# Kernel optimization log

Hardware: AMD Instinct MI355X
Metric: run time of the kernel (lower is better)

The kernel has to match this reference:

```python
import jax, jax.numpy as jnp
import numpy as np

N_NODES = 50000

def _spmm(edge_index, edge_weight, feat):
    # adj @ feat where adj is given as COO edge list (dst <- src)
    src = edge_index[1]
    dst = edge_index[0]
    msgs = feat[src] * edge_weight[:, None]  # [E, F]
    return jax.ops.segment_sum(msgs, dst, num_segments=N_NODES)

def setup_inputs() -> dict:
    key = jax.random.key(0)
    ks = jax.random.split(key, 8)
    E = 1600000
    x = jax.random.normal(ks[0], (N_NODES, 512), dtype=jnp.float32)
    edge_index = jax.random.randint(ks[1], (2, E), 0, N_NODES, dtype=jnp.int32)
    edge_weight = jax.random.uniform(ks[2], (E,), dtype=jnp.float32)
    # Glorot-ish init like GraphConvolution.reset_parameters
    W1 = jax.random.normal(ks[3], (512, 128), dtype=jnp.float32) / np.sqrt(512)
    b1 = jax.random.normal(ks[4], (128,), dtype=jnp.float32) * 0.01
    W2 = jax.random.normal(ks[5], (128, 64), dtype=jnp.float32) / np.sqrt(128)
    b2 = jax.random.normal(ks[6], (64,), dtype=jnp.float32) * 0.01
    return {"x": x, "edge_index": edge_index, "edge_weight": edge_weight,
            "W1": W1, "b1": b1, "W2": W2, "b2": b2}

def reference(x, edge_index, edge_weight, W1, b1, W2, b2):
    # eval mode: F.dropout is identity when not training
    # gc1: adj @ (x @ W1) + b1, then relu
    support1 = x @ W1                                   # [N, nhid]
    x1 = jax.nn.relu(_spmm(edge_index, edge_weight, support1) + b1)
    # gc2: adj @ (x1 @ W2) + b2
    support2 = x1 @ W2                                  # [N, out]
    x2 = _spmm(edge_index, edge_weight, support2) + b2
    return (x1, x2)
```

## Files before the change

kernel.cpp:

```cpp
#include <hip/hip_runtime.h>
#include <hip/hip_bf16.h>

#define N_NODES 50000
#define N_EDGES 1600000
#define F_IN    512
#define F_HID   128
#define F_OUT   64
#define NBUK    391
#define EPB     8192
#define CAP     4864

typedef short bf16x8 __attribute__((ext_vector_type(8)));
typedef float f32x4  __attribute__((ext_vector_type(4)));

__device__ __forceinline__ short f32_to_bf16(float f) {
    unsigned u = __float_as_uint(f);
    u += 0x7FFF + ((u >> 16) & 1);
    return (short)(u >> 16);
}
__device__ __forceinline__ float bf16_to_f32(short s) {
    return __uint_as_float(((unsigned)(unsigned short)s) << 16);
}
__device__ __forceinline__ float bf16lo(unsigned u) { return __uint_as_float(u << 16); }
__device__ __forceinline__ float bf16hi(unsigned u) { return __uint_as_float(u & 0xFFFF0000u); }

__device__ __forceinline__ bf16x8 cvt8(float4 lo, float4 hi) {
    union { unsigned u[4]; bf16x8 v; } r;
    asm("v_cvt_pk_bf16_f32 %0, %1, %2" : "=v"(r.u[0]) : "v"(lo.x), "v"(lo.y));
    asm("v_cvt_pk_bf16_f32 %0, %1, %2" : "=v"(r.u[1]) : "v"(lo.z), "v"(lo.w));
    asm("v_cvt_pk_bf16_f32 %0, %1, %2" : "=v"(r.u[2]) : "v"(hi.x), "v"(hi.y));
    asm("v_cvt_pk_bf16_f32 %0, %1, %2" : "=v"(r.u[3]) : "v"(hi.z), "v"(hi.w));
    return r.v;
}

__device__ __forceinline__ void gload16(const void* g, void* l) {
    __builtin_amdgcn_global_load_lds((const __attribute__((address_space(1))) void*)g,
                                     (__attribute__((address_space(3))) void*)l, 16, 0, 0);
}


__global__ __launch_bounds__(256) void part_a(const int* __restrict__ dst,
                                              const int* __restrict__ src,
                                              const float* __restrict__ w,
                                              int* __restrict__ gcnt,
                                              uint2* __restrict__ tmp, int E) {
    __shared__ int h[NBUK];
    __shared__ int base[NBUK];
    for (int i = threadIdx.x; i < NBUK; i += 256) h[i] = 0;
    __syncthreads();
    int e0 = blockIdx.x * EPB;
    int e1 = min(e0 + EPB, E);
    for (int e = e0 + threadIdx.x; e < e1; e += 256)
        atomicAdd(&h[dst[e] >> 7], 1);
    __syncthreads();
    for (int i = threadIdx.x; i < NBUK; i += 256) {
        int c = h[i];
        base[i] = c ? atomicAdd(&gcnt[i], c) : 0;
        h[i] = 0;
    }
    __syncthreads();
    for (int e = e0 + threadIdx.x; e < e1; e += 256) {
        int d = dst[e];
        int b = d >> 7;
        int off = base[b] + atomicAdd(&h[b], 1);
        if (off < CAP)
            tmp[(size_t)b * CAP + off] = make_uint2(((unsigned)d << 16) | (unsigned)src[e],
                                                    __float_as_uint(w[e]));
    }
}

__global__ __launch_bounds__(256) void part_b(const uint2* __restrict__ tmp,
                                              const int* __restrict__ gcnt,
                                              int2* __restrict__ rowinfo,
                                              uint2* __restrict__ erec) {
    __shared__ int s[128];
    __shared__ int cur[128];
    int b = blockIdx.x, tid = threadIdx.x;
    int nb0 = b << 7;
    int r0 = b * CAP;
    int cnt_b = min(gcnt[b], CAP);
    int r1 = r0 + cnt_b;
    if (tid < 128) s[tid] = 0;
    __syncthreads();
    for (int i = r0 + tid; i < r1; i += 256)
        atomicAdd(&s[(tmp[i].x >> 16) - nb0], 1);
    __syncthreads();
    int v = (tid < 128) ? s[tid] : 0;
    #pragma unroll
    for (int off = 1; off < 128; off <<= 1) {
        int t = (tid >= off && tid < 128) ? s[tid - off] : 0;
        __syncthreads();
        if (tid < 128) s[tid] += t;
        __syncthreads();
    }
    if (tid < 128) {
        int ex = r0 + s[tid] - v;
        cur[tid] = ex;
        int node = nb0 + tid;
        if (node < N_NODES) rowinfo[node] = make_int2(ex, ex + v);
    }
    __syncthreads();
    for (int i = r0 + tid; i < r1; i += 256) {
        uint2 rec = tmp[i];
        int p = atomicAdd(&cur[(rec.x >> 16) - nb0], 1);
        erec[p] = make_uint2(rec.x & 0xFFFFu, rec.y);
    }
}


template<int KD, int NC>
__global__ void wtrans_frag(const float* __restrict__ W, bf16x8* __restrict__ Bfrag) {
    constexpr int KC = KD / 32, NT = NC / 16;
    int u = blockIdx.x * 256 + threadIdx.x;
    if (u >= KC * NT * 64) return;
    int lane = u & 63;
    int nt   = (u >> 6) % NT;
    int kc   = u / (64 * NT);
    int n = nt * 16 + (lane & 15);
    int k = kc * 32 + (lane >> 4) * 8;
    bf16x8 f;
    #pragma unroll
    for (int j = 0; j < 8; ++j) f[j] = f32_to_bf16(W[(size_t)(k + j) * NC + n]);
    Bfrag[u] = f;
}

template<int KD , int NC >
__global__ __launch_bounds__(256) void mfma_gemm_s1(const float* __restrict__ X,
                                                    const bf16x8* __restrict__ Bfrag,
                                                    short* __restrict__ C, int Mrows) {
    constexpr int S = KD / 32;
    __shared__ char lds[2][16384];
    const int tid  = threadIdx.x;
    const int lane = tid & 63;
    const int wave = tid >> 6;
    const int wm = wave >> 1, wn = wave & 1;
    const int B0 = blockIdx.x * 64;
    const int r_lo = lane & 15, cg = lane >> 4;

    int rowA = B0 + wave * 16 + r_lo;
    if (rowA > Mrows - 1) rowA = Mrows - 1;
    const char* gA = (const char*)(X + (size_t)rowA * KD) + cg * 32;
    const char* gB = (const char*)Bfrag + (size_t)(wave * 2) * 1024 + (size_t)lane * 16;

    const int dA0 = (0 * 256 + wave * 64) * 16;
    const int dA1 = (1 * 256 + wave * 64) * 16;
    const int dB0 = 8192 + (wave * 2 + 0) * 1024;
    const int dB1 = 8192 + (wave * 2 + 1) * 1024;

    f32x4 acc[2][4];
    #pragma unroll
    for (int m = 0; m < 2; ++m)
        #pragma unroll
        for (int n = 0; n < 4; ++n) acc[m][n] = (f32x4){0.f, 0.f, 0.f, 0.f};

    {
        char* L = lds[0];
        gload16(gA,        L + dA0);
        gload16(gA + 16,   L + dA1);
        gload16(gB,        L + dB0);
        gload16(gB + 1024, L + dB1);
    }
    __syncthreads();

    int buf = 0;
    for (int s = 0; s < S; ++s) {
        if (s + 1 < S) {
            char* L = lds[buf ^ 1];
            const char* a = gA + (size_t)(s + 1) * 128;
            const char* b = gB + (size_t)(s + 1) * 8192;
            gload16(a,        L + dA0);
            gload16(a + 16,   L + dA1);
            gload16(b,        L + dB0);
            gload16(b + 1024, L + dB1);
        }
        const char* A_ = lds[buf];
        const char* B_ = lds[buf] + 8192;
        bf16x8 bb[4];
        #pragma unroll
        for (int n = 0; n < 4; ++n)
            bb[n] = *(const bf16x8*)(B_ + (wn * 4 + n) * 1024 + lane * 16);
        #pragma unroll
        for (int m = 0; m < 2; ++m) {
            int t = wm * 2 + m;
            float4 lo = *(const float4*)(A_ + (0 * 256 + t * 64 + lane) * 16);
            float4 hi = *(const float4*)(A_ + (1 * 256 + t * 64 + lane) * 16);
            bf16x8 a = cvt8(lo, hi);
            #pragma unroll
            for (int n = 0; n < 4; ++n)
                acc[m][n] = __builtin_amdgcn_mfma_f32_16x16x32_bf16(a, bb[n], acc[m][n], 0, 0, 0);
        }
        __syncthreads();
        buf ^= 1;
    }

    #pragma unroll
    for (int m = 0; m < 2; ++m) {
        int tile16 = (B0 >> 4) + wm * 2 + m;
        if (tile16 * 16 < Mrows) {
            #pragma unroll
            for (int n = 0; n < 4; ++n) {
                #pragma unroll
                for (int r = 0; r < 4; ++r) {
                    int grow = tile16 * 16 + cg * 4 + r;
                    C[(size_t)grow * NC + (wn * 4 + n) * 16 + r_lo] = f32_to_bf16(acc[m][n][r]);
                }
            }
        }
    }
}


template<int NC, int KD>
__global__ __launch_bounds__(256) void mfma_gemm_frag(const bf16x8* __restrict__ Afrag,
                                                      const bf16x8* __restrict__ Bfrag,
                                                      short* __restrict__ C, int Mt) {
    constexpr int NT = NC / 16, KC = KD / 32;
    constexpr int PFA = (KC < 4) ? KC : 4;
    const int lane = threadIdx.x & 63;
    const int wave = threadIdx.x >> 6;
    const int tile = blockIdx.x * 4 + wave;
    if (tile >= Mt) return;

    const bf16x8* ap = Afrag + (size_t)tile * KC * 64 + lane;
    const bf16x8* bp = Bfrag + lane;

    f32x4 acc[NT];
    #pragma unroll
    for (int i = 0; i < NT; ++i) acc[i] = (f32x4){0.f, 0.f, 0.f, 0.f};

    bf16x8 abuf[PFA];
    #pragma unroll
    for (int i = 0; i < PFA; ++i) abuf[i] = ap[(size_t)i * 64];
    bf16x8 bbuf[NT];
    #pragma unroll
    for (int nt = 0; nt < NT; ++nt) bbuf[nt] = bp[(size_t)nt * 64];

    #pragma unroll
    for (int kc = 0; kc < KC; ++kc) {
        bf16x8 a = abuf[kc % PFA];
        int ka = kc + PFA; if (ka > KC - 1) ka = KC - 1;
        abuf[kc % PFA] = ap[(size_t)ka * 64];
        int kb = (kc + 1 < KC) ? kc + 1 : kc;
        bf16x8 bnew[NT];
        #pragma unroll
        for (int nt = 0; nt < NT; ++nt) {
            bnew[nt] = bp[((size_t)kb * NT + nt) * 64];
            acc[nt] = __builtin_amdgcn_mfma_f32_16x16x32_bf16(a, bbuf[nt], acc[nt], 0, 0, 0);
        }
        #pragma unroll
        for (int nt = 0; nt < NT; ++nt) bbuf[nt] = bnew[nt];
    }

    const int lrow = lane & 15, kgrp = lane >> 4;
    #pragma unroll
    for (int nt = 0; nt < NT; ++nt) {
        #pragma unroll
        for (int r = 0; r < 4; ++r) {
            int grow = tile * 16 + kgrp * 4 + r;
            C[(size_t)grow * NC + nt * 16 + lrow] = f32_to_bf16(acc[nt][r]);
        }
    }
}


__global__ __launch_bounds__(64) void spmm128(const int2* __restrict__ rowinfo,
                                              const uint2* __restrict__ erec,
                                              const unsigned* __restrict__ featu,
                                              const float* __restrict__ bias,
                                              float* __restrict__ out,
                                              unsigned* __restrict__ afrag2u) {
    int d = blockIdx.x, tid = threadIdx.x;
    int2 ri = rowinfo[d];
    int beg = ri.x, end = ri.y;
    float a0 = 0.f, a1 = 0.f;
    const unsigned* fp = featu + tid;
    int e = beg;
    if (end - beg >= 8) {
        uint2 r[8];
        #pragma unroll
        for (int j = 0; j < 8; ++j) r[j] = erec[e + j];
        for (; e + 16 <= end; e += 8) {
            unsigned f[8];
            #pragma unroll
            for (int j = 0; j < 8; ++j) f[j] = fp[r[j].x * 64u];
            uint2 rn[8];
            #pragma unroll
            for (int j = 0; j < 8; ++j) rn[j] = erec[e + 8 + j];
            #pragma unroll
            for (int j = 0; j < 8; ++j) {
                float w = __uint_as_float(r[j].y);
                a0 += w * bf16lo(f[j]);
                a1 += w * bf16hi(f[j]);
            }
            #pragma unroll
            for (int j = 0; j < 8; ++j) r[j] = rn[j];
        }
        {
            unsigned f[8];
            #pragma unroll
            for (int j = 0; j < 8; ++j) f[j] = fp[r[j].x * 64u];
            #pragma unroll
            for (int j = 0; j < 8; ++j) {
                float w = __uint_as_float(r[j].y);
                a0 += w * bf16lo(f[j]);
                a1 += w * bf16hi(f[j]);
            }
            e += 8;
        }
    }
    for (; e + 4 <= end; e += 4) {
        uint2 r0 = erec[e], r1 = erec[e + 1], r2 = erec[e + 2], r3 = erec[e + 3];
        unsigned f0 = fp[r0.x * 64u];
        unsigned f1 = fp[r1.x * 64u];
        unsigned f2 = fp[r2.x * 64u];
        unsigned f3 = fp[r3.x * 64u];
        float w0 = __uint_as_float(r0.y), w1 = __uint_as_float(r1.y);
        float w2 = __uint_as_float(r2.y), w3 = __uint_as_float(r3.y);
        a0 += w0 * bf16lo(f0); a1 += w0 * bf16hi(f0);
        a0 += w1 * bf16lo(f1); a1 += w1 * bf16hi(f1);
        a0 += w2 * bf16lo(f2); a1 += w2 * bf16hi(f2);
        a0 += w3 * bf16lo(f3); a1 += w3 * bf16hi(f3);
    }
    for (; e < end; ++e) {
        uint2 r = erec[e];
        unsigned f = fp[r.x * 64u];
        float w = __uint_as_float(r.y);
        a0 += w * bf16lo(f); a1 += w * bf16hi(f);
    }
    float ox = fmaxf(a0 + bias[2 * tid], 0.f);
    float oy = fmaxf(a1 + bias[2 * tid + 1], 0.f);
    *(float2*)&out[(size_t)d * 128 + 2 * tid] = make_float2(ox, oy);
    unsigned packed = (unsigned)(unsigned short)f32_to_bf16(ox) |
                      ((unsigned)(unsigned short)f32_to_bf16(oy) << 16);
    int unit = ((d >> 4) * 4 + (tid >> 4)) * 64 + ((tid >> 2) & 3) * 16 + (d & 15);
    afrag2u[unit * 4 + (tid & 3)] = packed;
}

__global__ __launch_bounds__(64) void spmm64(const int2* __restrict__ rowinfo,
                                             const uint2* __restrict__ erec,
                                             const short* __restrict__ feat,
                                             const float* __restrict__ bias,
                                             float* __restrict__ out) {
    int d = blockIdx.x, tid = threadIdx.x;
    int2 ri = rowinfo[d];
    int beg = ri.x, end = ri.y;
    float acc = 0.f;
    const short* fp = feat + tid;
    int e = beg;
    if (end - beg >= 8) {
        uint2 r[8];
        #pragma unroll
        for (int j = 0; j < 8; ++j) r[j] = erec[e + j];
        for (; e + 16 <= end; e += 8) {
            float f[8];
            #pragma unroll
            for (int j = 0; j < 8; ++j) f[j] = bf16_to_f32(fp[r[j].x * 64u]);
            uint2 rn[8];
            #pragma unroll
            for (int j = 0; j < 8; ++j) rn[j] = erec[e + 8 + j];
            #pragma unroll
            for (int j = 0; j < 8; ++j) acc += __uint_as_float(r[j].y) * f[j];
            #pragma unroll
            for (int j = 0; j < 8; ++j) r[j] = rn[j];
        }
        {
            float f[8];
            #pragma unroll
            for (int j = 0; j < 8; ++j) f[j] = bf16_to_f32(fp[r[j].x * 64u]);
            #pragma unroll
            for (int j = 0; j < 8; ++j) acc += __uint_as_float(r[j].y) * f[j];
            e += 8;
        }
    }
    for (; e + 4 <= end; e += 4) {
        uint2 r0 = erec[e], r1 = erec[e + 1], r2 = erec[e + 2], r3 = erec[e + 3];
        float f0 = bf16_to_f32(fp[r0.x * 64u]);
        float f1 = bf16_to_f32(fp[r1.x * 64u]);
        float f2 = bf16_to_f32(fp[r2.x * 64u]);
        float f3 = bf16_to_f32(fp[r3.x * 64u]);
        acc += __uint_as_float(r0.y) * f0;
        acc += __uint_as_float(r1.y) * f1;
        acc += __uint_as_float(r2.y) * f2;
        acc += __uint_as_float(r3.y) * f3;
    }
    for (; e < end; ++e) {
        uint2 r = erec[e];
        acc += __uint_as_float(r.y) * bf16_to_f32(fp[r.x * 64u]);
    }
    out[(size_t)d * 64 + tid] = acc + bias[tid];
}


extern "C" void kernel_launch(void* const* d_in, const int* in_sizes, int n_in,
                              void* d_out, int out_size, void* d_ws, size_t ws_size,
                              hipStream_t stream) {
    const float* x  = (const float*)d_in[0];
    const int*   ei = (const int*)d_in[1];
    const float* ew = (const float*)d_in[2];
    const float* W1 = (const float*)d_in[3];
    const float* b1 = (const float*)d_in[4];
    const float* W2 = (const float*)d_in[5];
    const float* b2 = (const float*)d_in[6];

    const int* dst = ei;
    const int* src = ei + N_EDGES;

    float* x1 = (float*)d_out;
    float* x2 = x1 + (size_t)N_NODES * F_HID;

    char* ws = (char*)d_ws;
    uint2*  erec     = (uint2*)ws;  ws += (size_t)NBUK * CAP * 8;
    uint2*  tmp      = (uint2*)ws;  ws += (size_t)NBUK * CAP * 8;
    short*  support1 = (short*)ws;  ws += (size_t)N_NODES * F_HID * 2;
    short*  support2 = (short*)ws;  ws += (size_t)N_NODES * F_OUT * 2;
    bf16x8* Afrag2   = (bf16x8*)ws; ws += (size_t)N_NODES * F_HID * 2;
    bf16x8* Bfrag1   = (bf16x8*)ws; ws += (size_t)F_HID * F_IN * 2;
    bf16x8* Bfrag2   = (bf16x8*)ws; ws += (size_t)F_OUT * F_HID * 2;
    int2*   rowinfo  = (int2*)ws;   ws += (size_t)N_NODES * 8;
    int*    gcnt     = (int*)ws;    ws += 400 * 4;

    const int NPB = (N_EDGES + EPB - 1) / EPB;
    const int MT  = N_NODES / 16;

    hipMemsetAsync(gcnt, 0, NBUK * sizeof(int), stream);
    part_a<<<NPB, 256, 0, stream>>>(dst, src, ew, gcnt, tmp, N_EDGES);
    part_b<<<NBUK, 256, 0, stream>>>(tmp, gcnt, rowinfo, erec);

    wtrans_frag<F_IN, F_HID><<<32, 256, 0, stream>>>(W1, Bfrag1);
    wtrans_frag<F_HID, F_OUT><<<4, 256, 0, stream>>>(W2, Bfrag2);

    {
        int blocks = (N_NODES + 63) / 64;
        mfma_gemm_s1<F_IN, F_HID><<<blocks, 256, 0, stream>>>(x, Bfrag1, support1, N_NODES);
    }

    spmm128<<<N_NODES, 64, 0, stream>>>(rowinfo, erec, (const unsigned*)support1, b1, x1,
                                        (unsigned*)Afrag2);

    mfma_gemm_frag<F_OUT, F_HID><<<(MT + 3) / 4, 256, 0, stream>>>(Afrag2, Bfrag2, support2, MT);

    spmm64<<<N_NODES, 64, 0, stream>>>(rowinfo, erec, support2, b2, x2);
}
```

Measured before the change: 350.9 us.

## Triple-buffer GEMM LDS pipeline and merge weight-transform kernels

Replaces the double-buffered async global-to-LDS pipeline in the first GEMM with a three-stage ring, using explicit vmcnt waits and raw barriers so two stages of loads stay in flight during compute. It also merges the two weight-fragment conversion launches into a single kernel to save one launch. The LDS footprint per block grows from 32 KB to 48 KB, which may lower occupancy, and the hand-written waitcnt counts must match the number of loads issued per stage.

Result: no change. 349.2 us (-0.5%).

```diff
diff --git a/kernel.cpp b/kernel.cpp
--- a/kernel.cpp
+++ b/kernel.cpp
@@ -109,10 +109,9 @@
 
 
 template<int KD, int NC>
-__global__ void wtrans_frag(const float* __restrict__ W, bf16x8* __restrict__ Bfrag) {
-    constexpr int KC = KD / 32, NT = NC / 16;
-    int u = blockIdx.x * 256 + threadIdx.x;
-    if (u >= KC * NT * 64) return;
+__device__ __forceinline__ void wtrans_one(const float* __restrict__ W,
+                                           bf16x8* __restrict__ Bfrag, int u) {
+    constexpr int NT = NC / 16;
     int lane = u & 63;
     int nt   = (u >> 6) % NT;
     int kc   = u / (64 * NT);
@@ -124,12 +123,23 @@
     Bfrag[u] = f;
 }
 
+__global__ __launch_bounds__(256) void wtrans_all(const float* __restrict__ W1,
+                                                  const float* __restrict__ W2,
+                                                  bf16x8* __restrict__ B1,
+                                                  bf16x8* __restrict__ B2) {
+    constexpr int U1 = (F_IN / 32) * (F_HID / 16) * 64;
+    constexpr int U2 = (F_HID / 32) * (F_OUT / 16) * 64;
+    int u = blockIdx.x * 256 + threadIdx.x;
+    if (u < U1) wtrans_one<F_IN, F_HID>(W1, B1, u);
+    else if (u < U1 + U2) wtrans_one<F_HID, F_OUT>(W2, B2, u - U1);
+}
+
 template<int KD , int NC >
 __global__ __launch_bounds__(256) void mfma_gemm_s1(const float* __restrict__ X,
                                                     const bf16x8* __restrict__ Bfrag,
                                                     short* __restrict__ C, int Mrows) {
     constexpr int S = KD / 32;
-    __shared__ char lds[2][16384];
+    __shared__ char lds[3][16384];
     const int tid  = threadIdx.x;
     const int lane = tid & 63;
     const int wave = tid >> 6;
@@ -153,28 +163,17 @@
         #pragma unroll
         for (int n = 0; n < 4; ++n) acc[m][n] = (f32x4){0.f, 0.f, 0.f, 0.f};
 
-    {
-        char* L = lds[0];
-        gload16(gA,        L + dA0);
-        gload16(gA + 16,   L + dA1);
-        gload16(gB,        L + dB0);
-        gload16(gB + 1024, L + dB1);
-    }
-    __syncthreads();
-
-    int buf = 0;
-    for (int s = 0; s < S; ++s) {
-        if (s + 1 < S) {
-            char* L = lds[buf ^ 1];
-            const char* a = gA + (size_t)(s + 1) * 128;
-            const char* b = gB + (size_t)(s + 1) * 8192;
-            gload16(a,        L + dA0);
-            gload16(a + 16,   L + dA1);
-            gload16(b,        L + dB0);
-            gload16(b + 1024, L + dB1);
-        }
-        const char* A_ = lds[buf];
-        const char* B_ = lds[buf] + 8192;
+    auto issue_stage = [&](int s, char* L) {
+        const char* a = gA + (size_t)s * 128;
+        const char* b = gB + (size_t)s * 8192;
+        gload16(a,        L + dA0);
+        gload16(a + 16,   L + dA1);
+        gload16(b,        L + dB0);
+        gload16(b + 1024, L + dB1);
+    };
+    auto compute_step = [&](const char* L) {
+        const char* A_ = L;
+        const char* B_ = L + 8192;
         bf16x8 bb[4];
         #pragma unroll
         for (int n = 0; n < 4; ++n)
@@ -189,9 +188,25 @@
             for (int n = 0; n < 4; ++n)
                 acc[m][n] = __builtin_amdgcn_mfma_f32_16x16x32_bf16(a, bb[n], acc[m][n], 0, 0, 0);
         }
-        __syncthreads();
-        buf ^= 1;
-    }
+    };
+
+    issue_stage(0, lds[0]);
+    issue_stage(1, lds[1]);
+    issue_stage(2, lds[2]);
+
+    for (int s = 0; s < S - 2; ++s) {
+        asm volatile("s_waitcnt vmcnt(8)" ::: "memory");
+        asm volatile("s_barrier" ::: "memory");
+        compute_step(lds[s % 3]);
+        asm volatile("s_barrier" ::: "memory");
+        if (s + 3 < S) issue_stage(s + 3, lds[s % 3]);
+    }
+    asm volatile("s_waitcnt vmcnt(4)" ::: "memory");
+    asm volatile("s_barrier" ::: "memory");
+    compute_step(lds[(S - 2) % 3]);
+    asm volatile("s_waitcnt vmcnt(0)" ::: "memory");
+    asm volatile("s_barrier" ::: "memory");
+    compute_step(lds[(S - 1) % 3]);
 
     #pragma unroll
     for (int m = 0; m < 2; ++m) {
@@ -426,8 +441,7 @@
     part_a<<<NPB, 256, 0, stream>>>(dst, src, ew, gcnt, tmp, N_EDGES);
     part_b<<<NBUK, 256, 0, stream>>>(tmp, gcnt, rowinfo, erec);
 
-    wtrans_frag<F_IN, F_HID><<<32, 256, 0, stream>>>(W1, Bfrag1);
-    wtrans_frag<F_HID, F_OUT><<<4, 256, 0, stream>>>(W2, Bfrag2);
+    wtrans_all<<<36, 256, 0, stream>>>(W1, W2, Bfrag1, Bfrag2);
 
     {
         int blocks = (N_NODES + 63) / 64;
```
